# Performance work log

Hardware: AMD Instinct MI355X
Metric: run time of the kernel (lower is better)

The kernel has to match this reference:

```python
import jax, jax.numpy as jnp
import numpy as np

WINDOW = 512          # init window_size
OVERLAP = WINDOW // 4 # 128
FADE = OVERLAP // 2   # 64
ROPE_BASE = 10000.0


def _rope(x, pos):
    # x: (B,H,nw,W,D), pos: (nw,W) float
    D = x.shape[-1]
    inv_freq = 1.0 / (ROPE_BASE ** (jnp.arange(0, D, 2, dtype=jnp.float32) / D))
    ang = pos[..., None] * inv_freq                     # (nw,W,D/2)
    cos = jnp.concatenate([jnp.cos(ang), jnp.cos(ang)], -1)[None, None]  # (1,1,nw,W,D)
    sin = jnp.concatenate([jnp.sin(ang), jnp.sin(ang)], -1)[None, None]
    x1, x2 = x[..., : D // 2], x[..., D // 2 :]
    rot = jnp.concatenate([-x2, x1], -1)
    return x * cos + rot * sin


def setup_inputs() -> dict:
    key = jax.random.key(0)
    k1, k2, k3 = jax.random.split(key, 3)
    B, H, L, D = 2, 16, 8192, 64
    return {
        "query": jax.random.normal(k1, (B, H, L, D), jnp.float32),
        "key": jax.random.normal(k2, (B, H, L, D), jnp.float32),
        "value": jax.random.normal(k3, (B, H, L, D), jnp.float32),
        "position_ids": jnp.arange(L, dtype=jnp.int64),
    }


def reference(query, key, value, position_ids):
    B, H, L, D = query.shape
    nw = L // WINDOW
    qw = query.reshape(B, H, nw, WINDOW, D)
    kw = key.reshape(B, H, nw, WINDOW, D)
    vw = value.reshape(B, H, nw, WINDOW, D)
    pos = position_ids.reshape(nw, WINDOW).astype(jnp.float32)

    q = _rope(qw, pos)
    k = _rope(kw, pos)

    scores = jnp.einsum("bhnqd,bhnkd->bhnqk", q, k) / jnp.sqrt(jnp.float32(D))
    attn = jax.nn.softmax(scores, axis=-1)
    win_out = jnp.einsum("bhnqk,bhnkd->bhnqd", attn, vw)  # (B,H,nw,W,D)

    # overlap-fade blend weights per window (middle windows fade at edges;
    # first/last windows use full weight). out = win_out * w / (w + 1e-8).
    fade_in = jnp.linspace(0.0, 1.0, FADE)
    fade_out = jnp.linspace(1.0, 0.0, FADE)
    w_mid = jnp.concatenate([fade_in, jnp.ones(WINDOW - 2 * FADE), fade_out])
    w_edge = jnp.ones(WINDOW)
    idx = jnp.arange(nw)
    is_edge = (idx == 0) | (idx == nw - 1)
    w = jnp.where(is_edge[:, None], w_edge[None, :], w_mid[None, :])  # (nw,W)
    scale = (w / (w + 1e-8))[None, None, :, :, None]
    out = win_out * scale
    return out.reshape(B, H, L, D)
```

## Files before the change

kernel.cpp:

```cpp
#include <hip/hip_runtime.h>

typedef _Float16 half8 __attribute__((ext_vector_type(8)));
typedef _Float16 half4 __attribute__((ext_vector_type(4)));
typedef _Float16 half2v __attribute__((ext_vector_type(2)));
typedef float floatx4 __attribute__((ext_vector_type(4)));
typedef float floatx2 __attribute__((ext_vector_type(2)));

#define MFMA_F16 __builtin_amdgcn_mfma_f32_16x16x32_f16
#define FREQ (-0.41524101186092f)

static __device__ __forceinline__ unsigned pack_f16(float a, float b) {
    half2v h; h.x = (_Float16)a; h.y = (_Float16)b;
    return __builtin_bit_cast(unsigned, h);
}

__global__ __launch_bounds__(512, 4) void swa6(
    const float* __restrict__ Q, const float* __restrict__ K,
    const float* __restrict__ V, const int* __restrict__ pid,
    float* __restrict__ Out)
{
    __shared__ __align__(16) _Float16 lq[128 * 72];
    __shared__ __align__(16) _Float16 lk[2][32 * 64];
    __shared__ __align__(16) _Float16 lvt[2][64 * 32];

    const int bid   = blockIdx.x;
    const int half_ = (bid >> 3) & 1;
    const int win   = (bid & 7) | ((bid >> 4) << 3);
    const int n = win & 15, bh = win >> 4;
    const long long winrow = (long long)bh * 8192 + n * 512;
    const long long qbase  = winrow + half_ * 256;
    const float* Qb = Q + qbase * 64;
    const float* Kb = K + winrow * 64;
    const float* Vb = V + winrow * 64;
    float* Ob = Out + qbase * 64;
    const int pidq = n * 512 + half_ * 256;
    const int pidk = n * 512;

    const int tid = threadIdx.x, lane = tid & 63, wv = tid >> 6;
    const int l15 = lane & 15, quad = (lane >> 4) & 3;
    const float CS = 0.125f * 1.44269504088896f;

    half8 qf[2][2];
    {
        const int rowl = tid >> 2;
        const int dq   = (tid & 3) * 8;
        float ifq[8];
        #pragma unroll
        for (int i = 0; i < 8; ++i) ifq[i] = __builtin_exp2f((float)(dq + i) * FREQ);
        for (int rnd = 0; rnd < 2; ++rnd) {
            const float* src = Qb + (rnd * 128 + rowl) * 64;
            float pos = (float)pid[pidq + rnd * 128 + rowl];
            float4 a0 = *(const float4*)(src + dq);
            float4 a1 = *(const float4*)(src + dq + 4);
            float4 b0 = *(const float4*)(src + 32 + dq);
            float4 b1 = *(const float4*)(src + 36 + dq);
            float lo[8] = {a0.x,a0.y,a0.z,a0.w,a1.x,a1.y,a1.z,a1.w};
            float hi[8] = {b0.x,b0.y,b0.z,b0.w,b1.x,b1.y,b1.z,b1.w};
            half8 wlo, whi;
            #pragma unroll
            for (int i = 0; i < 8; ++i) {
                float sn, cn;
                __sincosf(pos * ifq[i], &sn, &cn);
                wlo[i] = (_Float16)((lo[i] * cn - hi[i] * sn) * CS);
                whi[i] = (_Float16)((hi[i] * cn + lo[i] * sn) * CS);
            }
            if (rnd) __syncthreads();
            *(half8*)&lq[rowl * 72 + dq]      = wlo;
            *(half8*)&lq[rowl * 72 + 32 + dq] = whi;
            __syncthreads();
            if ((wv >> 2) == rnd) {
                const int rb = (wv & 3) * 32;
                #pragma unroll
                for (int rt = 0; rt < 2; ++rt) {
                    qf[rt][0] = *(const half8*)&lq[(rb + rt * 16 + l15) * 72 + quad * 8];
                    qf[rt][1] = *(const half8*)&lq[(rb + rt * 16 + l15) * 72 + 32 + quad * 8];
                }
            }
        }
    }

    floatx4 o[2][4], ol[2];
    #pragma unroll
    for (int rt = 0; rt < 2; ++rt) {
        ol[rt] = (floatx4){0.f, 0.f, 0.f, 0.f};
        #pragma unroll
        for (int vt = 0; vt < 4; ++vt) o[rt][vt] = (floatx4){0.f, 0.f, 0.f, 0.f};
    }
    half8 onesf;
    #pragma unroll
    for (int i = 0; i < 8; ++i) onesf[i] = (_Float16)1.0f;

    const int key = tid >> 4;
    const int pr  = tid & 15;
    const int dv  = tid & 63;
    const int grp = tid >> 6;
    float if2[2];
    #pragma unroll
    for (int i = 0; i < 2; ++i) if2[i] = __builtin_exp2f((float)(pr * 2 + i) * FREQ);
    const int klo_addr = key * 64 + (((pr >> 2) ^ (key & 7)) * 8) + (pr & 3) * 2;
    const int khi_addr = key * 64 + ((((pr >> 2) + 4) ^ (key & 7)) * 8) + (pr & 3) * 2;
    const int vst_addr = dv * 32 + (((grp & 3) ^ ((dv >> 1) & 3)) * 8) + (grp >> 2) * 4;
    const int ksw0 = (quad ^ (l15 & 7)) * 8;
    const int ksw1 = ((quad + 4) ^ (l15 & 7)) * 8;
    const int vsw  = (quad ^ ((l15 >> 1) & 3)) * 8;

    floatx2 ka  = *(const floatx2*)(Kb + key * 64 + pr * 2);
    floatx2 kb2 = *(const floatx2*)(Kb + key * 64 + 32 + pr * 2);
    float vr[4];
    #pragma unroll
    for (int i = 0; i < 4; ++i) vr[i] = Vb[(grp * 4 + i) * 64 + dv];
    int kp = pid[pidk + key];

    for (int kc = 0; kc < 16; ++kc) {
        const int cur = kc & 1;
        float kpos = (float)kp;
        half2v klo, khi;
        {
            float a[2] = {ka.x, ka.y};
            float b[2] = {kb2.x, kb2.y};
            #pragma unroll
            for (int i = 0; i < 2; ++i) {
                float sn, cn;
                __sincosf(kpos * if2[i], &sn, &cn);
                klo[i] = (_Float16)(a[i] * cn - b[i] * sn);
                khi[i] = (_Float16)(b[i] * cn + a[i] * sn);
            }
        }
        half4 vh;
        #pragma unroll
        for (int i = 0; i < 4; ++i) vh[i] = (_Float16)vr[i];

        *(half2v*)&lk[cur][klo_addr] = klo;
        *(half2v*)&lk[cur][khi_addr] = khi;
        *(half4*)&lvt[cur][vst_addr] = vh;
        __syncthreads();

        if (kc < 15) {
            const float* kn = Kb + (kc + 1) * 2048;
            const float* vn = Vb + (kc + 1) * 2048;
            ka  = *(const floatx2*)(kn + key * 64 + pr * 2);
            kb2 = *(const floatx2*)(kn + key * 64 + 32 + pr * 2);
            #pragma unroll
            for (int i = 0; i < 4; ++i) vr[i] = vn[(grp * 4 + i) * 64 + dv];
            kp = pid[pidk + (kc + 1) * 32 + key];
        }

        half8 kf00 = *(const half8*)&lk[cur][l15 * 64 + ksw0];
        half8 kf01 = *(const half8*)&lk[cur][l15 * 64 + ksw1];
        half8 kf10 = *(const half8*)&lk[cur][(16 + l15) * 64 + ksw0];
        half8 kf11 = *(const half8*)&lk[cur][(16 + l15) * 64 + ksw1];
        half8 vf[4];
        #pragma unroll
        for (int vt = 0; vt < 4; ++vt)
            vf[vt] = *(const half8*)&lvt[cur][(vt * 16 + l15) * 32 + vsw];

        __builtin_amdgcn_s_setprio(1);
        #pragma unroll
        for (int rt = 0; rt < 2; ++rt) {
            floatx4 s0 = {0.f,0.f,0.f,0.f}, s1 = {0.f,0.f,0.f,0.f};
            s0 = MFMA_F16(kf00, qf[rt][0], s0, 0, 0, 0);
            s0 = MFMA_F16(kf01, qf[rt][1], s0, 0, 0, 0);
            s1 = MFMA_F16(kf10, qf[rt][0], s1, 0, 0, 0);
            s1 = MFMA_F16(kf11, qf[rt][1], s1, 0, 0, 0);

            union { unsigned u[4]; half8 h; } pfu;
            pfu.u[0] = pack_f16(__builtin_exp2f(s0[0]), __builtin_exp2f(s0[1]));
            pfu.u[1] = pack_f16(__builtin_exp2f(s0[2]), __builtin_exp2f(s0[3]));
            pfu.u[2] = pack_f16(__builtin_exp2f(s1[0]), __builtin_exp2f(s1[1]));
            pfu.u[3] = pack_f16(__builtin_exp2f(s1[2]), __builtin_exp2f(s1[3]));
            half8 pf = pfu.h;

            ol[rt] = MFMA_F16(pf, onesf, ol[rt], 0, 0, 0);
            #pragma unroll
            for (int vt = 0; vt < 4; ++vt)
                o[rt][vt] = MFMA_F16(pf, vf[vt], o[rt][vt], 0, 0, 0);
        }
        __builtin_amdgcn_s_setprio(0);
    }

    #pragma unroll
    for (int rt = 0; rt < 2; ++rt) {
        #pragma unroll
        for (int r = 0; r < 4; ++r) {
            int rowl = wv * 32 + rt * 16 + quad * 4 + r;
            int j = half_ * 256 + rowl;
            float w;
            if (n == 0 || n == 15)  w = 1.0f;
            else if (j < 64)        w = (float)j * (1.0f / 63.0f);
            else if (j >= 448)      w = (float)(511 - j) * (1.0f / 63.0f);
            else                    w = 1.0f;
            float f = (w / (w + 1e-8f)) / ol[rt][r];
            #pragma unroll
            for (int vt = 0; vt < 4; ++vt)
                Ob[rowl * 64 + vt * 16 + l15] = o[rt][vt][r] * f;
        }
    }
}

extern "C" void kernel_launch(void* const* d_in, const int* in_sizes, int n_in,
                              void* d_out, int out_size, void* d_ws, size_t ws_size,
                              hipStream_t stream) {
    const float* q   = (const float*)d_in[0];
    const float* k   = (const float*)d_in[1];
    const float* v   = (const float*)d_in[2];
    const int*   pid = (const int*)d_in[3];
    float* out = (float*)d_out;
    (void)in_sizes; (void)n_in; (void)out_size; (void)d_ws; (void)ws_size;
    swa6<<<dim3(1024), dim3(512), 0, stream>>>(q, k, v, pid, out);
}
```

Before: 234.5 us.

## Split each window's queries across four 256-thread blocks instead of two

Each block now handles 128 query rows (a quarter window) with 256 threads, so the grid doubles to 2048 blocks. Each thread stages K/V chunks into LDS with wider loads: float4 K loads with four rope rotations, and eight V rows per thread. The aim is finer-grained scheduling and better occupancy balance across CUs, plus fewer, wider load instructions per thread. The cost is that every K/V window is now loaded and roped by four blocks instead of two, doubling redundant K/V traffic and rope work.

Measured after the change: 280.2 us. 1.19x slower.

```diff
diff --git a/kernel.cpp b/kernel.cpp
--- a/kernel.cpp
+++ b/kernel.cpp
@@ -4,7 +4,6 @@
 typedef _Float16 half4 __attribute__((ext_vector_type(4)));
 typedef _Float16 half2v __attribute__((ext_vector_type(2)));
 typedef float floatx4 __attribute__((ext_vector_type(4)));
-typedef float floatx2 __attribute__((ext_vector_type(2)));
 
 #define MFMA_F16 __builtin_amdgcn_mfma_f32_16x16x32_f16
 #define FREQ (-0.41524101186092f)
@@ -14,26 +13,26 @@
     return __builtin_bit_cast(unsigned, h);
 }
 
-__global__ __launch_bounds__(512, 4) void swa6(
+__global__ __launch_bounds__(256, 4) void swa8(
     const float* __restrict__ Q, const float* __restrict__ K,
     const float* __restrict__ V, const int* __restrict__ pid,
     float* __restrict__ Out)
 {
-    __shared__ __align__(16) _Float16 lq[128 * 72];
+    __shared__ __align__(16) _Float16 lq[64 * 72];
     __shared__ __align__(16) _Float16 lk[2][32 * 64];
     __shared__ __align__(16) _Float16 lvt[2][64 * 32];
 
-    const int bid   = blockIdx.x;
-    const int half_ = (bid >> 3) & 1;
-    const int win   = (bid & 7) | ((bid >> 4) << 3);
+    const int bid     = blockIdx.x;
+    const int quarter = (bid >> 3) & 3;
+    const int win     = (bid & 7) | ((bid >> 5) << 3);
     const int n = win & 15, bh = win >> 4;
     const long long winrow = (long long)bh * 8192 + n * 512;
-    const long long qbase  = winrow + half_ * 256;
+    const long long qbase  = winrow + quarter * 128;
     const float* Qb = Q + qbase * 64;
     const float* Kb = K + winrow * 64;
     const float* Vb = V + winrow * 64;
     float* Ob = Out + qbase * 64;
-    const int pidq = n * 512 + half_ * 256;
+    const int pidq = n * 512 + quarter * 128;
     const int pidk = n * 512;
 
     const int tid = threadIdx.x, lane = tid & 63, wv = tid >> 6;
@@ -48,8 +47,8 @@
         #pragma unroll
         for (int i = 0; i < 8; ++i) ifq[i] = __builtin_exp2f((float)(dq + i) * FREQ);
         for (int rnd = 0; rnd < 2; ++rnd) {
-            const float* src = Qb + (rnd * 128 + rowl) * 64;
-            float pos = (float)pid[pidq + rnd * 128 + rowl];
+            const float* src = Qb + (rnd * 64 + rowl) * 64;
+            float pos = (float)pid[pidq + rnd * 64 + rowl];
             float4 a0 = *(const float4*)(src + dq);
             float4 a1 = *(const float4*)(src + dq + 4);
             float4 b0 = *(const float4*)(src + 32 + dq);
@@ -68,8 +67,8 @@
             *(half8*)&lq[rowl * 72 + dq]      = wlo;
             *(half8*)&lq[rowl * 72 + 32 + dq] = whi;
             __syncthreads();
-            if ((wv >> 2) == rnd) {
-                const int rb = (wv & 3) * 32;
+            if ((wv >> 1) == rnd) {
+                const int rb = (wv & 1) * 32;
                 #pragma unroll
                 for (int rt = 0; rt < 2; ++rt) {
                     qf[rt][0] = *(const half8*)&lq[(rb + rt * 16 + l15) * 72 + quad * 8];
@@ -90,58 +89,64 @@
     #pragma unroll
     for (int i = 0; i < 8; ++i) onesf[i] = (_Float16)1.0f;
 
-    const int key = tid >> 4;
-    const int pr  = tid & 15;
+    const int key = tid >> 3;
+    const int d0  = (tid & 7) * 4;
     const int dv  = tid & 63;
-    const int grp = tid >> 6;
-    float if2[2];
-    #pragma unroll
-    for (int i = 0; i < 2; ++i) if2[i] = __builtin_exp2f((float)(pr * 2 + i) * FREQ);
-    const int klo_addr = key * 64 + (((pr >> 2) ^ (key & 7)) * 8) + (pr & 3) * 2;
-    const int khi_addr = key * 64 + ((((pr >> 2) + 4) ^ (key & 7)) * 8) + (pr & 3) * 2;
-    const int vst_addr = dv * 32 + (((grp & 3) ^ ((dv >> 1) & 3)) * 8) + (grp >> 2) * 4;
+    const int k8  = tid >> 6;
+    float if4[4];
+    #pragma unroll
+    for (int i = 0; i < 4; ++i) if4[i] = __builtin_exp2f((float)(d0 + i) * FREQ);
+    const int klo_addr = key * 64 + (((d0 >> 3) ^ (key & 7)) * 8) + (d0 & 7);
+    const int khi_addr = key * 64 + ((((d0 >> 3) + 4) ^ (key & 7)) * 8) + (d0 & 7);
+    int vst_addr[2];
+    #pragma unroll
+    for (int h = 0; h < 2; ++h) {
+        int g = 2 * k8 + h;
+        vst_addr[h] = dv * 32 + (((g & 3) ^ ((dv >> 1) & 3)) * 8) + ((g >> 2) * 4);
+    }
     const int ksw0 = (quad ^ (l15 & 7)) * 8;
     const int ksw1 = ((quad + 4) ^ (l15 & 7)) * 8;
     const int vsw  = (quad ^ ((l15 >> 1) & 3)) * 8;
 
-    floatx2 ka  = *(const floatx2*)(Kb + key * 64 + pr * 2);
-    floatx2 kb2 = *(const floatx2*)(Kb + key * 64 + 32 + pr * 2);
-    float vr[4];
-    #pragma unroll
-    for (int i = 0; i < 4; ++i) vr[i] = Vb[(grp * 4 + i) * 64 + dv];
+    float4 ka  = *(const float4*)(Kb + key * 64 + d0);
+    float4 kb2 = *(const float4*)(Kb + key * 64 + 32 + d0);
+    float vr[8];
+    #pragma unroll
+    for (int i = 0; i < 8; ++i) vr[i] = Vb[(k8 * 8 + i) * 64 + dv];
     int kp = pid[pidk + key];
 
     for (int kc = 0; kc < 16; ++kc) {
         const int cur = kc & 1;
         float kpos = (float)kp;
-        half2v klo, khi;
+        half4 klo, khi;
         {
-            float a[2] = {ka.x, ka.y};
-            float b[2] = {kb2.x, kb2.y};
-            #pragma unroll
-            for (int i = 0; i < 2; ++i) {
+            float a[4] = {ka.x, ka.y, ka.z, ka.w};
+            float b[4] = {kb2.x, kb2.y, kb2.z, kb2.w};
+            #pragma unroll
+            for (int i = 0; i < 4; ++i) {
                 float sn, cn;
-                __sincosf(kpos * if2[i], &sn, &cn);
+                __sincosf(kpos * if4[i], &sn, &cn);
                 klo[i] = (_Float16)(a[i] * cn - b[i] * sn);
                 khi[i] = (_Float16)(b[i] * cn + a[i] * sn);
             }
         }
-        half4 vh;
-        #pragma unroll
-        for (int i = 0; i < 4; ++i) vh[i] = (_Float16)vr[i];
-
-        *(half2v*)&lk[cur][klo_addr] = klo;
-        *(half2v*)&lk[cur][khi_addr] = khi;
-        *(half4*)&lvt[cur][vst_addr] = vh;
+        half4 vh0, vh1;
+        #pragma unroll
+        for (int i = 0; i < 4; ++i) { vh0[i] = (_Float16)vr[i]; vh1[i] = (_Float16)vr[4 + i]; }
+
+        *(half4*)&lk[cur][klo_addr] = klo;
+        *(half4*)&lk[cur][khi_addr] = khi;
+        *(half4*)&lvt[cur][vst_addr[0]] = vh0;
+        *(half4*)&lvt[cur][vst_addr[1]] = vh1;
         __syncthreads();
 
         if (kc < 15) {
             const float* kn = Kb + (kc + 1) * 2048;
             const float* vn = Vb + (kc + 1) * 2048;
-            ka  = *(const floatx2*)(kn + key * 64 + pr * 2);
-            kb2 = *(const floatx2*)(kn + key * 64 + 32 + pr * 2);
-            #pragma unroll
-            for (int i = 0; i < 4; ++i) vr[i] = vn[(grp * 4 + i) * 64 + dv];
+            ka  = *(const float4*)(kn + key * 64 + d0);
+            kb2 = *(const float4*)(kn + key * 64 + 32 + d0);
+            #pragma unroll
+            for (int i = 0; i < 8; ++i) vr[i] = vn[(k8 * 8 + i) * 64 + dv];
             kp = pid[pidk + (kc + 1) * 32 + key];
         }
 
@@ -183,7 +188,7 @@
         #pragma unroll
         for (int r = 0; r < 4; ++r) {
             int rowl = wv * 32 + rt * 16 + quad * 4 + r;
-            int j = half_ * 256 + rowl;
+            int j = quarter * 128 + rowl;
             float w;
             if (n == 0 || n == 15)  w = 1.0f;
             else if (j < 64)        w = (float)j * (1.0f / 63.0f);
@@ -206,5 +211,5 @@
     const int*   pid = (const int*)d_in[3];
     float* out = (float*)d_out;
     (void)in_sizes; (void)n_in; (void)out_size; (void)d_ws; (void)ws_size;
-    swa6<<<dim3(1024), dim3(512), 0, stream>>>(q, k, v, pid, out);
+    swa8<<<dim3(2048), dim3(256), 0, stream>>>(q, k, v, pid, out);
 }
```
